# Performance work log

Measured on AMD Instinct MI355X. Metric: run time of the kernel, lower is better.

The kernel has to match this reference:

```python
import jax, jax.numpy as jnp
import numpy as np

K = 20  # max_similar_relations


def setup_inputs() -> dict:
    key = jax.random.key(0)
    k1, k2 = jax.random.split(key)
    B, R, D = 256, 2048, 64
    x = jax.random.normal(k1, (B, R, D), dtype=jnp.float32)
    query_rels = jax.random.randint(k2, (B,), 0, R, dtype=jnp.int32)
    return {
        "x": x,
        "query_rels": query_rels,
        # raw params as in __init__: threshold_init=0.2 -> raw=0.2*2-1=-0.6; strength_init=0.05 -> raw=0.05*5-1=-0.75
        "threshold_raw": jnp.float32(-0.6),
        "strength_raw": jnp.float32(-0.75),
        "weight_scale": jnp.float32(1.0),
        "temperature": jnp.float32(1.0),
    }


def reference(x, query_rels, threshold_raw, strength_raw, weight_scale, temperature):
    B, R, D = x.shape
    bidx = jnp.arange(B)
    threshold = jax.nn.sigmoid(threshold_raw)
    strength = jax.nn.sigmoid(strength_raw) * 0.2
    temp = jnp.clip(temperature, 0.1, 10.0)

    # F.normalize(x, p=2, dim=2)
    norms = x / jnp.maximum(jnp.linalg.norm(x, axis=2, keepdims=True), 1e-12)

    q = norms[bidx, query_rels]                      # [B, D] normalized query reprs
    sims = jnp.einsum("bd,brd->br", q, norms)        # [B, R] cosine similarities
    sims = sims.at[bidx, query_rels].set(-1.0)       # exclude self
    sim_w = jax.nn.sigmoid((sims - threshold) * 10.0)

    topv, topi = jax.lax.top_k(sims, K)              # [B, K]
    valid = (topv > threshold) & (topi != query_rels[:, None])

    # softmax over valid top-k entries only (per batch row)
    logits = jnp.where(valid, topv / temp, -1e9)
    w = jax.nn.softmax(logits, axis=1)
    w = jnp.where(valid, w, 0.0)

    sw = jnp.take_along_axis(sim_w, topi, axis=1)    # smooth sigmoid weights of selected
    combined = w * sw
    adjusted = combined * (1.0 + weight_scale * topv)
    adjusted = adjusted / (jnp.sum(adjusted, axis=1, keepdims=True) + 1e-8)

    # gather top-k normalized reprs and weighted-sum them
    top_reprs = jnp.take_along_axis(norms, jnp.broadcast_to(topi[:, :, None], (B, K, D)), axis=1)
    weighted = jnp.einsum("bk,bkd->bd", adjusted, top_reprs)  # [B, D]

    q_orig = x[bidx, query_rels]                     # original (unnormalized) query repr
    has_valid = jnp.any(valid, axis=1, keepdims=True)
    mixed = (1.0 - strength) * q_orig + strength * weighted
    new_q = jnp.where(has_valid, mixed, q_orig)

    return x.at[bidx, query_rels].set(new_q)
```

## Files before the change

kernel.cpp:

```cpp
#include <hip/hip_runtime.h>
#include <math.h>

#define KTOP 20
#define R_MAX 2048

__global__ __launch_bounds__(1024) void fused_enhancer(
    const float* __restrict__ x,
    const int* __restrict__ qrels,
    const float* __restrict__ thr_raw,
    const float* __restrict__ str_raw,
    const float* __restrict__ wscale_p,
    const float* __restrict__ temp_p,
    float* __restrict__ out, int R)
{
    __shared__ float s_q[64];
    __shared__ float s_sims[R_MAX];
    __shared__ float s_dn[R_MAX];
    __shared__ int   s_cand[R_MAX];
    __shared__ int   s_ncand;
    __shared__ float s_topv[KTOP];
    __shared__ int   s_topi[KTOP];
    __shared__ float s_adj[KTOP];
    __shared__ float s_strength;

    const int b = blockIdx.x;
    const int t = threadIdx.x;
    const int qr = qrels[b];
    const float threshold = 1.0f / (1.0f + expf(-thr_raw[0]));

    if (t == 0) s_ncand = 0;

    if (t < 64) {
        float v = x[((long)b * R + qr) * 64 + t];
        float ss = v * v;
#pragma unroll
        for (int m = 1; m < 64; m <<= 1) ss += __shfl_xor(ss, m, 64);
        s_q[t] = v / fmaxf(sqrtf(ss), 1e-12f);
    }
    __syncthreads();

    const int grp = t >> 4, l16 = t & 15;
    const float4 q4 = *(const float4*)(s_q + l16 * 4);
    const long xbase = (long)b * R * 64;
    for (int row = grp; row < R; row += 64) {
        long base = xbase + (long)row * 64 + l16 * 4;
        const float4 v = *(const float4*)(x + base);
        *(float4*)(out + base) = v;
        float dot = v.x * q4.x + v.y * q4.y + v.z * q4.z + v.w * q4.w;
        float ss  = v.x * v.x + v.y * v.y + v.z * v.z + v.w * v.w;
#pragma unroll
        for (int m = 1; m < 16; m <<= 1) {
            dot += __shfl_xor(dot, m, 64);
            ss  += __shfl_xor(ss,  m, 64);
        }
        if (l16 == 0) {
            float dn  = fmaxf(sqrtf(ss), 1e-12f);
            float sim = (row == qr) ? -1.0f : dot / dn;
            s_sims[row] = sim;
            s_dn[row]   = dn;
            if (sim > threshold) {
                int p = atomicAdd(&s_ncand, 1);
                s_cand[p] = row;
            }
        }
    }
    __syncthreads();

    const int ncand = s_ncand;
    const int ksel = ncand < KTOP ? ncand : KTOP;

    if (t < 64) {
        if (ncand > KTOP) {
            float lv[32]; int li[32];
#pragma unroll
            for (int j = 0; j < 32; ++j) {
                int i = t + 64 * j;
                if (i < ncand) { li[j] = s_cand[i]; lv[j] = s_sims[li[j]]; }
                else           { li[j] = 0x7fffffff; lv[j] = -INFINITY; }
            }
            for (int k = 0; k < KTOP; ++k) {
                float bv = -INFINITY; int bi = 0x7fffffff;
#pragma unroll
                for (int j = 0; j < 32; ++j) {
                    if (lv[j] > bv || (lv[j] == bv && li[j] < bi)) { bv = lv[j]; bi = li[j]; }
                }
#pragma unroll
                for (int m = 1; m < 64; m <<= 1) {
                    float v2 = __shfl_xor(bv, m, 64);
                    int   i2 = __shfl_xor(bi, m, 64);
                    if (v2 > bv || (v2 == bv && i2 < bi)) { bv = v2; bi = i2; }
                }
#pragma unroll
                for (int j = 0; j < 32; ++j) if (li[j] == bi) lv[j] = -INFINITY;
                if (t == 0) { s_topv[k] = bv; s_topi[k] = bi; }
            }
        } else if (t == 0) {
            for (int k = 0; k < ksel; ++k) {
                int idx = s_cand[k];
                s_topi[k] = idx;
                s_topv[k] = s_sims[idx];
            }
        }
    }

    if (t == 0) {
        float strength = (1.0f / (1.0f + expf(-str_raw[0]))) * 0.2f;
        float temp = fminf(fmaxf(temp_p[0], 0.1f), 10.0f);
        float wsc  = wscale_p[0];
        if (ksel > 0) {
            float m = -INFINITY;
            for (int k = 0; k < ksel; ++k) m = fmaxf(m, s_topv[k] / temp);
            float w[KTOP]; float wsum = 0.0f;
            for (int k = 0; k < ksel; ++k) { w[k] = expf(s_topv[k] / temp - m); wsum += w[k]; }
            float adj[KTOP]; float asum = 0.0f;
            for (int k = 0; k < ksel; ++k) {
                float tv = s_topv[k];
                float sw = 1.0f / (1.0f + expf(-(tv - threshold) * 10.0f));
                float a  = (w[k] / wsum) * sw * (1.0f + wsc * tv);
                adj[k] = a; asum += a;
            }
            for (int k = 0; k < ksel; ++k)
                s_adj[k] = (adj[k] / (asum + 1e-8f)) / s_dn[s_topi[k]];
        }
        s_strength = strength;
    }
    __syncthreads();

    if (t < 64 && ksel > 0) {
        long qb = ((long)b * R + qr) * 64 + t;
        float qo = x[qb];
        float acc = 0.0f;
        for (int k = 0; k < ksel; ++k)
            acc += s_adj[k] * x[((long)b * R + s_topi[k]) * 64 + t];
        float st = s_strength;
        out[qb] = (1.0f - st) * qo + st * acc;
    }
}

extern "C" void kernel_launch(void* const* d_in, const int* in_sizes, int n_in,
                              void* d_out, int out_size, void* d_ws, size_t ws_size,
                              hipStream_t stream) {
    const float* x      = (const float*)d_in[0];
    const int*   qrels  = (const int*)d_in[1];
    const float* thr    = (const float*)d_in[2];
    const float* str    = (const float*)d_in[3];
    const float* wscale = (const float*)d_in[4];
    const float* temp   = (const float*)d_in[5];
    float* out = (float*)d_out;

    const int B = in_sizes[1];
    const int D = 64;
    const int R = in_sizes[0] / (B * D);
    (void)D; (void)d_ws; (void)ws_size;

    fused_enhancer<<<B, 1024, 0, stream>>>(x, qrels, thr, str, wscale, temp, out, R);
}
```

Baseline: 253.8 us.

## Split fused kernel into parallel streaming-sims pass and per-row select/mix pass

Replaces the single 1024-thread-per-batch kernel with two kernels. The first spreads each batch row's 2048 relations over 8 blocks of 256 threads, streams x into out with nontemporal stores, processes two rows per thread group, and writes similarities and norms to workspace. The second reloads the similarities per batch, compacts the candidates, runs top-k, and does the weighted mix. The aim is more blocks and better occupancy for the memory-bound copy, at the cost of an extra launch and a workspace round-trip. The old fused kernel is kept as a fallback when the workspace is too small or the shape doesn't fit.

```diff
diff --git a/kernel.cpp b/kernel.cpp
--- a/kernel.cpp
+++ b/kernel.cpp
@@ -3,6 +3,186 @@
 
 #define KTOP 20
 #define R_MAX 2048
+#define SPLIT 8
+
+typedef float f4v __attribute__((ext_vector_type(4)));
+
+__global__ __launch_bounds__(256, 6) void stream_sims(
+    const float* __restrict__ x,
+    const int* __restrict__ qrels,
+    float* __restrict__ out,
+    float* __restrict__ sims,
+    float* __restrict__ dns,
+    int R)
+{
+    __shared__ float s_q[64];
+    const int blk = blockIdx.x;
+    const int b = blk >> 3;
+    const int s = blk & (SPLIT - 1);
+    const int t = threadIdx.x;
+    const int qr = qrels[b];
+    const long xbase = (long)b * R * 64;
+
+    if (t < 64) {
+        float v = x[xbase + (long)qr * 64 + t];
+        float ss = v * v;
+#pragma unroll
+        for (int m = 1; m < 64; m <<= 1) ss += __shfl_xor(ss, m, 64);
+        s_q[t] = v / fmaxf(sqrtf(ss), 1e-12f);
+    }
+    __syncthreads();
+
+    const int grp = t >> 4, l16 = t & 15;
+    const float4 q4 = *(const float4*)(s_q + l16 * 4);
+    const int rpb = R / SPLIT;
+    const int row0 = s * rpb;
+    const long sbase = (long)b * R;
+
+    for (int r = row0 + grp; r < row0 + rpb; r += 32) {
+        const int rA = r, rB = r + 16;
+        const long baseA = xbase + (long)rA * 64 + l16 * 4;
+        const long baseB = xbase + (long)rB * 64 + l16 * 4;
+        const float4 vA = *(const float4*)(x + baseA);
+        const float4 vB = *(const float4*)(x + baseB);
+        __builtin_nontemporal_store(*(const f4v*)&vA, (f4v*)(out + baseA));
+        __builtin_nontemporal_store(*(const f4v*)&vB, (f4v*)(out + baseB));
+
+        float dotA = vA.x * q4.x + vA.y * q4.y + vA.z * q4.z + vA.w * q4.w;
+        float ssA  = vA.x * vA.x + vA.y * vA.y + vA.z * vA.z + vA.w * vA.w;
+        float dotB = vB.x * q4.x + vB.y * q4.y + vB.z * q4.z + vB.w * q4.w;
+        float ssB  = vB.x * vB.x + vB.y * vB.y + vB.z * vB.z + vB.w * vB.w;
+#pragma unroll
+        for (int m = 1; m < 16; m <<= 1) {
+            dotA += __shfl_xor(dotA, m, 64);
+            ssA  += __shfl_xor(ssA,  m, 64);
+            dotB += __shfl_xor(dotB, m, 64);
+            ssB  += __shfl_xor(ssB,  m, 64);
+        }
+        if (l16 == 0) {
+            float dnA = fmaxf(sqrtf(ssA), 1e-12f);
+            float dnB = fmaxf(sqrtf(ssB), 1e-12f);
+            sims[sbase + rA] = (rA == qr) ? -1.0f : dotA / dnA;
+            sims[sbase + rB] = (rB == qr) ? -1.0f : dotB / dnB;
+            dns[sbase + rA] = dnA;
+            dns[sbase + rB] = dnB;
+        }
+    }
+}
+
+__global__ __launch_bounds__(256) void select_mix(
+    const float* __restrict__ x,
+    const int* __restrict__ qrels,
+    const float* __restrict__ thr_raw,
+    const float* __restrict__ str_raw,
+    const float* __restrict__ wscale_p,
+    const float* __restrict__ temp_p,
+    const float* __restrict__ sims,
+    const float* __restrict__ dns,
+    float* __restrict__ out,
+    int R)
+{
+    __shared__ float s_sims[R_MAX];
+    __shared__ int   s_cand[R_MAX];
+    __shared__ int   s_ncand;
+    __shared__ float s_topv[KTOP];
+    __shared__ int   s_topi[KTOP];
+    __shared__ float s_dnsel[KTOP];
+    __shared__ float s_adj[KTOP];
+    __shared__ float s_strength;
+
+    const int b = blockIdx.x;
+    const int t = threadIdx.x;
+    const int qr = qrels[b];
+    const float threshold = 1.0f / (1.0f + expf(-thr_raw[0]));
+    const long sbase = (long)b * R;
+    const long xbase = (long)b * R * 64;
+
+    if (t == 0) s_ncand = 0;
+    __syncthreads();
+
+    for (int i = t; i < R; i += 256) {
+        float sv = sims[sbase + i];
+        s_sims[i] = sv;
+        if (sv > threshold) {
+            int p = atomicAdd(&s_ncand, 1);
+            s_cand[p] = i;
+        }
+    }
+    __syncthreads();
+
+    const int ncand = s_ncand;
+    const int ksel = ncand < KTOP ? ncand : KTOP;
+
+    if (t < 64) {
+        float myv = 0.0f; int myi = 0;
+        if (ncand > KTOP) {
+            float lv[32]; int li[32];
+#pragma unroll
+            for (int j = 0; j < 32; ++j) {
+                int i = t + 64 * j;
+                if (i < ncand) { li[j] = s_cand[i]; lv[j] = s_sims[li[j]]; }
+                else           { li[j] = 0x7fffffff; lv[j] = -INFINITY; }
+            }
+            for (int k = 0; k < KTOP; ++k) {
+                float bv = -INFINITY; int bi = 0x7fffffff;
+#pragma unroll
+                for (int j = 0; j < 32; ++j)
+                    if (lv[j] > bv || (lv[j] == bv && li[j] < bi)) { bv = lv[j]; bi = li[j]; }
+#pragma unroll
+                for (int m = 1; m < 64; m <<= 1) {
+                    float v2 = __shfl_xor(bv, m, 64);
+                    int   i2 = __shfl_xor(bi, m, 64);
+                    if (v2 > bv || (v2 == bv && i2 < bi)) { bv = v2; bi = i2; }
+                }
+#pragma unroll
+                for (int j = 0; j < 32; ++j) if (li[j] == bi) lv[j] = -INFINITY;
+                if (t == k) { myv = bv; myi = bi; }
+            }
+        } else if (t < ksel) {
+            myi = s_cand[t];
+            myv = s_sims[myi];
+        }
+        if (t < ksel) {
+            s_topv[t] = myv;
+            s_topi[t] = myi;
+            s_dnsel[t] = dns[sbase + myi];
+        }
+    }
+    __syncthreads();
+
+    if (t == 0) {
+        float strength = (1.0f / (1.0f + expf(-str_raw[0]))) * 0.2f;
+        float temp = fminf(fmaxf(temp_p[0], 0.1f), 10.0f);
+        float wsc  = wscale_p[0];
+        if (ksel > 0) {
+            float m = -INFINITY;
+            for (int k = 0; k < ksel; ++k) m = fmaxf(m, s_topv[k] / temp);
+            float w[KTOP]; float wsum = 0.0f;
+            for (int k = 0; k < ksel; ++k) { w[k] = expf(s_topv[k] / temp - m); wsum += w[k]; }
+            float adj[KTOP]; float asum = 0.0f;
+            for (int k = 0; k < ksel; ++k) {
+                float tv = s_topv[k];
+                float sw = 1.0f / (1.0f + expf(-(tv - threshold) * 10.0f));
+                float a  = (w[k] / wsum) * sw * (1.0f + wsc * tv);
+                adj[k] = a; asum += a;
+            }
+            for (int k = 0; k < ksel; ++k)
+                s_adj[k] = (adj[k] / (asum + 1e-8f)) / s_dnsel[k];
+        }
+        s_strength = strength;
+    }
+    __syncthreads();
+
+    if (t < 64 && ksel > 0) {
+        const long qb = xbase + (long)qr * 64 + t;
+        float qo = x[qb];
+        float acc = 0.0f;
+        for (int k = 0; k < ksel; ++k)
+            acc += s_adj[k] * x[xbase + (long)s_topi[k] * 64 + t];
+        float st = s_strength;
+        out[qb] = (1.0f - st) * qo + st * acc;
+    }
+}
 
 __global__ __launch_bounds__(1024) void fused_enhancer(
     const float* __restrict__ x,
@@ -151,7 +331,16 @@
     const int B = in_sizes[1];
     const int D = 64;
     const int R = in_sizes[0] / (B * D);
-    (void)D; (void)d_ws; (void)ws_size;
-
-    fused_enhancer<<<B, 1024, 0, stream>>>(x, qrels, thr, str, wscale, temp, out, R);
+    (void)D;
+
+    const size_t need = (size_t)B * R * 2 * sizeof(float);
+    if (d_ws != nullptr && ws_size >= need && (R % (SPLIT * 32)) == 0 && R <= R_MAX) {
+        float* sims = (float*)d_ws;
+        float* dns  = sims + (size_t)B * R;
+        stream_sims<<<B * SPLIT, 256, 0, stream>>>(x, qrels, out, sims, dns, R);
+        select_mix<<<B, 256, 0, stream>>>(x, qrels, thr, str, wscale, temp,
+                                          sims, dns, out, R);
+    } else {
+        fused_enhancer<<<B, 1024, 0, stream>>>(x, qrels, thr, str, wscale, temp, out, R);
+    }
 }
```

New measurement: 258.2 us. About the same (+1.7%).
